# Kernel optimization log

Measured on AMD Instinct MI355X. Metric: run time of the kernel, lower is better.

The kernel has to match this reference:

```python
import jax, jax.numpy as jnp
import numpy as np

D = 1024
N_HEADS = 16


def build_masks(H, W):
    # Row-major grid: token i -> (i // W, i % W). True = attend.
    idx = jnp.arange(H * W)
    r, c = idx // W, idx % W
    ri, rj = r[:, None], r[None, :]
    ci, cj = c[:, None], c[None, :]
    lr = (ri > rj) | ((ri == rj) & (ci >= cj))
    rl = (ri < rj) | ((ri == rj) & (ci <= cj))
    td = (ci > cj) | ((ci == cj) & (ri >= rj))
    bu = (ci < cj) | ((ci == cj) & (ri <= rj))
    return lr, rl, td, bu


def dir_attn(x, w_qkv, w_o, mask):
    # x: (B,T,D); w_qkv: (3D,D); w_o: (D,D); mask: (T,T) bool
    B, T, Dm = x.shape
    hd = Dm // N_HEADS
    qkv = (x @ w_qkv.T).reshape(B, T, 3, N_HEADS, hd)
    q = qkv[:, :, 0].transpose(0, 2, 1, 3)  # (B,H,T,hd)
    k = qkv[:, :, 1].transpose(0, 2, 1, 3)
    v = qkv[:, :, 2].transpose(0, 2, 1, 3)
    scores = jnp.einsum('bhqd,bhkd->bhqk', q, k) / np.sqrt(hd)
    scores = jnp.where(mask[None, None], scores, -jnp.inf)
    attn = jax.nn.softmax(scores, axis=-1)
    y = jnp.einsum('bhqk,bhkd->bhqd', attn, v)
    y = y.transpose(0, 2, 1, 3).reshape(B, T, Dm)
    return y @ w_o.T


def rmsnorm(x, w, eps=1e-6):
    norm = jax.lax.rsqrt(jnp.mean(jnp.square(x.astype(jnp.float32)), axis=-1, keepdims=True) + eps)
    return (x.astype(jnp.float32) * norm).astype(x.dtype) * w


def setup_inputs() -> dict:
    key = jax.random.key(0)
    ks = jax.random.split(key, 13)
    s = 0.02
    inp = {
        'x': jax.random.normal(ks[0], (4, 1024, D), dtype=jnp.float32),
        'w_qkv_lr': jax.random.normal(ks[1], (3 * D, D), dtype=jnp.float32) * s,
        'w_o_lr':   jax.random.normal(ks[2], (D, D), dtype=jnp.float32) * s,
        'w_qkv_rl': jax.random.normal(ks[3], (3 * D, D), dtype=jnp.float32) * s,
        'w_o_rl':   jax.random.normal(ks[4], (D, D), dtype=jnp.float32) * s,
        'w_qkv_td': jax.random.normal(ks[5], (3 * D, D), dtype=jnp.float32) * s,
        'w_o_td':   jax.random.normal(ks[6], (D, D), dtype=jnp.float32) * s,
        'w_qkv_bu': jax.random.normal(ks[7], (3 * D, D), dtype=jnp.float32) * s,
        'w_o_bu':   jax.random.normal(ks[8], (D, D), dtype=jnp.float32) * s,
        'w_gate':   jax.random.normal(ks[9], (4 * D, 4 * D), dtype=jnp.float32) * s,
        'b_gate':   jnp.zeros((4 * D,), dtype=jnp.float32),
        'w_out':    jax.random.normal(ks[10], (D, 4 * D), dtype=jnp.float32) * s,
        'norm_w':   jnp.ones((D,), dtype=jnp.float32),
        'grid_h': 32,
        'grid_w': 32,
    }
    return inp


def reference(x, w_qkv_lr, w_o_lr, w_qkv_rl, w_o_rl, w_qkv_td, w_o_td,
              w_qkv_bu, w_o_bu, w_gate, b_gate, w_out, norm_w, grid_h, grid_w):
    m_lr, m_rl, m_td, m_bu = build_masks(grid_h, grid_w)
    h_lr = dir_attn(x, w_qkv_lr, w_o_lr, m_lr)
    h_rl = dir_attn(x, w_qkv_rl, w_o_rl, m_rl)
    h_td = dir_attn(x, w_qkv_td, w_o_td, m_td)
    h_bu = dir_attn(x, w_qkv_bu, w_o_bu, m_bu)
    concat = jnp.concatenate([h_lr, h_rl, h_td, h_bu], axis=-1)  # (B,T,4D)
    gate = jax.nn.sigmoid(concat @ w_gate.T + b_gate)
    fused = (gate * concat) @ w_out.T
    return rmsnorm(fused + x, norm_w)
```

## Files before the change

### kernel.cpp

```cpp
#include <hip/hip_runtime.h>
#include <hip/hip_bf16.h>
#include <math.h>


typedef __bf16 bf16_t;
typedef __bf16 bf16x4 __attribute__((ext_vector_type(4)));
typedef __bf16 bf16x8 __attribute__((ext_vector_type(8)));
typedef float  f32x4  __attribute__((ext_vector_type(4)));

#define MFMA16(a, b, c) __builtin_amdgcn_mfma_f32_16x16x32_bf16((a), (b), (c), 0, 0, 0)

__device__ __forceinline__ void async16(const bf16_t* g, bf16_t* l) {
  __builtin_amdgcn_global_load_lds((const __attribute__((address_space(1))) void*)g,
                                   (__attribute__((address_space(3))) void*)l,
                                   16, 0, 0);
}

__device__ __forceinline__ float dpp_max16(float x) {
  float t;
  t = __builtin_bit_cast(float, __builtin_amdgcn_update_dpp(0, __builtin_bit_cast(int, x), 0xB1, 0xF, 0xF, true));
  x = fmaxf(x, t);
  t = __builtin_bit_cast(float, __builtin_amdgcn_update_dpp(0, __builtin_bit_cast(int, x), 0x4E, 0xF, 0xF, true));
  x = fmaxf(x, t);
  t = __builtin_bit_cast(float, __builtin_amdgcn_update_dpp(0, __builtin_bit_cast(int, x), 0x124, 0xF, 0xF, true));
  x = fmaxf(x, t);
  t = __builtin_bit_cast(float, __builtin_amdgcn_update_dpp(0, __builtin_bit_cast(int, x), 0x128, 0xF, 0xF, true));
  x = fmaxf(x, t);
  return x;
}
__device__ __forceinline__ float dpp_sum16(float x) {
  float t;
  t = __builtin_bit_cast(float, __builtin_amdgcn_update_dpp(0, __builtin_bit_cast(int, x), 0xB1, 0xF, 0xF, true));
  x += t;
  t = __builtin_bit_cast(float, __builtin_amdgcn_update_dpp(0, __builtin_bit_cast(int, x), 0x4E, 0xF, 0xF, true));
  x += t;
  t = __builtin_bit_cast(float, __builtin_amdgcn_update_dpp(0, __builtin_bit_cast(int, x), 0x124, 0xF, 0xF, true));
  x += t;
  t = __builtin_bit_cast(float, __builtin_amdgcn_update_dpp(0, __builtin_bit_cast(int, x), 0x128, 0xF, 0xF, true));
  x += t;
  return x;
}

struct Ptr4 { const bf16_t* p[4]; };

__device__ __forceinline__ int perm_t(int p, int dir) {
  int q = (dir & 1) ? (1023 - p) : p;
  if (dir >= 2) q = ((q & 31) << 5) | (q >> 5);
  return q;
}

struct CvtDesc {
  const float* src[9];
  bf16_t* dst[9];
  int n8[9];
};

__device__ __forceinline__ void cvt8(const float* in, bf16_t* out, int i) {
  const float4 a = ((const float4*)in)[i * 2];
  const float4 b = ((const float4*)in)[i * 2 + 1];
  bf16x8 o;
  o[0] = (bf16_t)a.x; o[1] = (bf16_t)a.y; o[2] = (bf16_t)a.z; o[3] = (bf16_t)a.w;
  o[4] = (bf16_t)b.x; o[5] = (bf16_t)b.y; o[6] = (bf16_t)b.z; o[7] = (bf16_t)b.w;
  ((bf16x8*)out)[i] = o;
}

__global__ __launch_bounds__(256) void cvt9_k(CvtDesc d) {
  const int seg = blockIdx.y;
  const int i = blockIdx.x * 256 + threadIdx.x;
  if (i >= d.n8[seg]) return;
  cvt8(d.src[seg], d.dst[seg], i);
}

template <int MODE>
__global__ __launch_bounds__(512, 2) void gemm_bt2(
    const bf16_t* __restrict__ A, long sAz, int lda,
    Ptr4 B4, int ldb,
    void* __restrict__ Cv, long sCz, int ldc, int K, int koff,
    const float* __restrict__ bias,
    const bf16_t* __restrict__ gin,
    bf16_t* __restrict__ vtp, long sVz, int dirbase) {
  constexpr int BM = 256, BN = 256, BK = 64;
  (void)BM; (void)BN;
  __shared__ __align__(16) char smem[131072];

  const int z = blockIdx.z;
  const bf16_t* Ap = A + (long)z * sAz;
  const bf16_t* Bp = B4.p[z];
  const int tid = threadIdx.x;
  const int lane = tid & 63;
  const int wave = tid >> 6;
  const int l15 = lane & 15, qd = lane >> 4;
  const int wm = wave >> 2, wn = wave & 3;
  const int bm = blockIdx.y * 256, bn = blockIdx.x * 256;
  const int kz = (MODE == 3) ? z * koff : 0;
  const int NT = K / BK;

  const int row0 = tid >> 3;
  const int blkp = ((tid & 7) ^ (row0 & 7)) * 8;
  const bf16_t* gA = Ap + (long)(bm + row0) * lda + blkp + kz;
  const bf16_t* gB = Bp + (long)(bn + row0) * ldb + blkp + kz;
  char* const sm = (char*)smem;
  const int ldsT = tid * 16;

  const int xorv = (l15 & 7) << 4;
  const int aBase = (wm * 128 + l15) * 128;
  const int bBase = 32768 + (wn * 64 + l15) * 128;
  const int colk0 = (qd * 16) ^ xorv;
  const int colk1 = (64 + qd * 16) ^ xorv;

  f32x4 acc[8][4];
#pragma unroll
  for (int i = 0; i < 8; i++)
#pragma unroll
    for (int j = 0; j < 4; j++) acc[i][j] = (f32x4){0.f, 0.f, 0.f, 0.f};

#pragma unroll
  for (int u = 0; u < 4; u++)
    async16(gA + (long)(u * 64) * lda, (bf16_t*)(sm + u * 8192 + ldsT));
#pragma unroll
  for (int u = 0; u < 4; u++)
    async16(gB + (long)(u * 64) * ldb, (bf16_t*)(sm + 32768 + u * 8192 + ldsT));
  asm volatile("s_waitcnt vmcnt(0)" ::: "memory");
  __builtin_amdgcn_s_barrier();

  for (int kt = 0; kt < NT; ++kt) {
    const int c = kt & 1;
    const char* sa = sm + c * 65536;
    const int nb = (c ^ 1) * 65536;
    const long ko = (long)(kt + 1) * BK;
    bf16x8 bF[4][2];
#pragma unroll
    for (int p = 0; p < 4; ++p) {
      if (p == 0) {
#pragma unroll
        for (int n = 0; n < 4; ++n) {
          bF[n][0] = *(const bf16x8*)(sa + bBase + n * 2048 + colk0);
          bF[n][1] = *(const bf16x8*)(sa + bBase + n * 2048 + colk1);
        }
      }
      bf16x8 aF[2][2];
#pragma unroll
      for (int mm = 0; mm < 2; ++mm) {
        aF[mm][0] = *(const bf16x8*)(sa + aBase + (p * 2 + mm) * 2048 + colk0);
        aF[mm][1] = *(const bf16x8*)(sa + aBase + (p * 2 + mm) * 2048 + colk1);
      }
      if (kt + 1 < NT) {
        if (p == 0) {
#pragma unroll
          for (int u = 0; u < 4; u++)
            async16(gA + (long)(u * 64) * lda + ko,
                    (bf16_t*)(sm + nb + u * 8192 + ldsT));
        } else if (p == 1) {
#pragma unroll
          for (int u = 0; u < 4; u++)
            async16(gB + (long)(u * 64) * ldb + ko,
                    (bf16_t*)(sm + nb + 32768 + u * 8192 + ldsT));
        }
      }
      __builtin_amdgcn_s_barrier();
      asm volatile("s_waitcnt lgkmcnt(0)" ::: "memory");
      __builtin_amdgcn_s_setprio(1);
#pragma unroll
      for (int kh = 0; kh < 2; ++kh)
#pragma unroll
        for (int mm = 0; mm < 2; ++mm)
#pragma unroll
          for (int n = 0; n < 4; ++n)
            acc[p * 2 + mm][n] =
                MFMA16(aF[mm][kh], bF[n][kh], acc[p * 2 + mm][n]);
      __builtin_amdgcn_s_setprio(0);
      if (p == 3 && kt + 1 < NT)
        asm volatile("s_waitcnt vmcnt(0)" ::: "memory");
      __builtin_amdgcn_s_barrier();
    }
  }

  if constexpr (MODE == 4) {
    const int dir = dirbase + z;
    if (bn < 2048) {
      bf16_t* qkz = (bf16_t*)Cv + (long)z * sCz;
      const float ksc = (bn >= 1024) ? 0.125f : 1.0f;
      float* sC = (float*)smem;
#pragma unroll
      for (int p = 0; p < 4; ++p) {
        if (p) __syncthreads();
        if (wm == (p >> 1)) {
#pragma unroll
          for (int mm = 0; mm < 4; ++mm) {
            const int m = (p & 1) * 4 + mm;
#pragma unroll
            for (int n = 0; n < 4; ++n)
#pragma unroll
              for (int r = 0; r < 4; ++r)
                sC[(mm * 16 + qd * 4 + r) * 260 + wn * 64 + n * 16 + l15] =
                    acc[m][n][r];
          }
        }
        __syncthreads();
#pragma unroll
        for (int i = 0; i < 8; ++i) {
          const int idx = i * 512 + tid;
          const int rl = idx >> 6, c4 = (idx & 63) * 4;
          const float4 v4 = *(const float4*)&sC[rl * 260 + c4];
          const int grow = bm + p * 64 + rl;
          const int prow = (grow & ~1023) | perm_t(grow & 1023, dir);
          bf16x4 o;
          o[0] = (bf16_t)(v4.x * ksc); o[1] = (bf16_t)(v4.y * ksc);
          o[2] = (bf16_t)(v4.z * ksc); o[3] = (bf16_t)(v4.w * ksc);
          *(bf16x4*)(qkz + (long)prow * ldc + bn + c4) = o;
        }
      }
    } else if (dir < 2) {
      bf16_t* vz = vtp + (long)z * sVz;
      float* sCt = (float*)smem;
#pragma unroll
      for (int p = 0; p < 4; ++p) {
        if (p) __syncthreads();
        if (wm == (p >> 1)) {
#pragma unroll
          for (int mm = 0; mm < 4; ++mm) {
            const int m = (p & 1) * 4 + mm;
#pragma unroll
            for (int n = 0; n < 4; ++n)
#pragma unroll
              for (int r = 0; r < 4; ++r)
                sCt[(wn * 64 + n * 16 + l15) * 68 + mm * 16 + qd * 4 + r] =
                    acc[m][n][r];
          }
        }
        __syncthreads();
#pragma unroll
        for (int i = 0; i < 8; ++i) {
          const int idx = i * 512 + tid;
          const int col = idx >> 4, tq = idx & 15;
          const float4 v4 = *(const float4*)&sCt[col * 68 + tq * 4];
          const int t0 = (bm & 1023) + p * 64 + tq * 4;
          const int bb = bm >> 10;
          const int ch = bn + col - 2048;
          bf16_t* vrow =
              vz + (((long)bb * 16 + (ch >> 6)) * 64 + (ch & 63)) * 1024;
          if (dir == 0) {
            bf16x4 o;
            o[0] = (bf16_t)v4.x; o[1] = (bf16_t)v4.y;
            o[2] = (bf16_t)v4.z; o[3] = (bf16_t)v4.w;
            *(bf16x4*)(vrow + t0) = o;
          } else {
            bf16x4 o;
            o[0] = (bf16_t)v4.w; o[1] = (bf16_t)v4.z;
            o[2] = (bf16_t)v4.y; o[3] = (bf16_t)v4.x;
            *(bf16x4*)(vrow + (1020 - t0)) = o;
          }
        }
      }
    } else {
      bf16_t* vz = vtp + (long)z * sVz;
      bf16_t* sV = (bf16_t*)smem;
      const int bmm = bm & 1023;
      const int bb = bm >> 10;
      const int ub5 = ((dir & 1) ? (768 - bmm) : bmm) >> 5;
#pragma unroll
      for (int h = 0; h < 2; ++h) {
        if (h) __syncthreads();
        if ((wn >> 1) == h) {
          const int colB = (wn & 1) * 64;
#pragma unroll
          for (int m = 0; m < 8; ++m)
#pragma unroll
            for (int n = 0; n < 4; ++n)
#pragma unroll
              for (int r = 0; r < 4; ++r) {
                const int t = bmm + wm * 128 + m * 16 + qd * 4 + r;
                const int u = (dir & 1) ? (1023 - t) : t;
                const int cpi = (u & 31) * 8 + ((u >> 5) & 7);
                sV[(colB + n * 16 + l15) * 264 + cpi] = (bf16_t)acc[m][n][r];
              }
        }
        __syncthreads();
#pragma unroll
        for (int i = 0; i < 8; ++i) {
          const int idx = i * 512 + tid;
          const int col = idx >> 5, cg = idx & 31;
          const bf16x8 v = *(const bf16x8*)&sV[col * 264 + cg * 8];
          const int ch = bn + h * 128 + col - 2048;
          bf16_t* vrow =
              vz + (((long)bb * 16 + (ch >> 6)) * 64 + (ch & 63)) * 1024;
          *(bf16x8*)(vrow + cg * 32 + ub5) = v;
        }
      }
    }
  } else {
    float* sC = (float*)smem;
#pragma unroll
    for (int p = 0; p < 4; ++p) {
      if (p) __syncthreads();
      if (wm == (p >> 1)) {
#pragma unroll
        for (int mm = 0; mm < 4; ++mm) {
          const int m = (p & 1) * 4 + mm;
#pragma unroll
          for (int n = 0; n < 4; ++n)
#pragma unroll
            for (int r = 0; r < 4; ++r)
              sC[(mm * 16 + qd * 4 + r) * 260 + wn * 64 + n * 16 + l15] =
                  acc[m][n][r];
        }
      }
      __syncthreads();
#pragma unroll
      for (int i = 0; i < 8; ++i) {
        const int idx = i * 512 + tid;
        const int rl = idx >> 6, c4 = (idx & 63) * 4;
        const float4 v4 = *(const float4*)&sC[rl * 260 + c4];
        const int grow = bm + p * 64 + rl;
        const int gcol = bn + c4;
        const long goff = (long)grow * ldc + gcol;
        if constexpr (MODE == 0) {
          bf16x4 o;
          o[0] = (bf16_t)v4.x; o[1] = (bf16_t)v4.y;
          o[2] = (bf16_t)v4.z; o[3] = (bf16_t)v4.w;
          *(bf16x4*)((bf16_t*)Cv + (long)z * sCz + goff) = o;
        } else if constexpr (MODE == 1) {
          const float4 bb = *(const float4*)&bias[gcol];
          const bf16x4 gv = *(const bf16x4*)&gin[goff];
          bf16x4 o;
          o[0] = (bf16_t)((float)gv[0] / (1.f + __expf(-(v4.x + bb.x))));
          o[1] = (bf16_t)((float)gv[1] / (1.f + __expf(-(v4.y + bb.y))));
          o[2] = (bf16_t)((float)gv[2] / (1.f + __expf(-(v4.z + bb.z))));
          o[3] = (bf16_t)((float)gv[3] / (1.f + __expf(-(v4.w + bb.w))));
          *(bf16x4*)((bf16_t*)Cv + goff) = o;
        } else {
          *(float4*)((float*)Cv + (long)z * sCz + goff) = v4;
        }
      }
    }
  }
}

template <int MODE>
__global__ __launch_bounds__(256) void gemm_bt(
    const bf16_t* __restrict__ A, long sAz, int lda,
    Ptr4 B4, int ldb,
    void* __restrict__ Cv, long sCz, int ldc, int K, int koff,
    const float* __restrict__ bias,
    const bf16_t* __restrict__ gin,
    bf16_t* __restrict__ vtp, long sVz, int dirbase) {
  constexpr int BM = 128, BN = 128, BK = 32;
  __shared__ __align__(16) char smem[18432];
  bf16_t* sA = (bf16_t*)smem;
  bf16_t* sB = (bf16_t*)(smem + BM * BK * 2);
  float* sC = (float*)smem;

  const int z = blockIdx.z;
  const bf16_t* Ap = A + (long)z * sAz;
  const bf16_t* Bp = B4.p[z];
  const int tid = threadIdx.x;
  const int wave = tid >> 6, lane = tid & 63;
  const int lane15 = lane & 15, quad = lane >> 4;
  const int bm = blockIdx.y * BM, bn = blockIdx.x * BN;
  const int wm = (wave >> 1) * 64, wn = (wave & 1) * 64;

  f32x4 acc[4][4];
#pragma unroll
  for (int i = 0; i < 4; i++)
#pragma unroll
    for (int j = 0; j < 4; j++) acc[i][j] = (f32x4){0.f, 0.f, 0.f, 0.f};

  const int srow = wave * 16 + (lane >> 2);
  const int skoff = (lane & 3) * 8;
  const int kz = (MODE == 3) ? z * koff : 0;
  const bf16_t* ga = Ap + (long)(bm + srow) * lda + skoff + kz;
  const bf16_t* gb = Bp + (long)(bn + srow) * ldb + skoff + kz;
  bf16_t* la = &sA[srow * BK + skoff];
  bf16_t* lb = &sB[srow * BK + skoff];

  for (int k0 = 0; k0 < K; k0 += BK) {
    __syncthreads();
    async16(ga + k0, la);
    async16(ga + k0 + (long)64 * lda, la + 64 * BK);
    async16(gb + k0, lb);
    async16(gb + k0 + (long)64 * ldb, lb + 64 * BK);
    __syncthreads();

    bf16x8 af[4], bfv[4];
#pragma unroll
    for (int i = 0; i < 4; i++)
      af[i] = *(const bf16x8*)&sA[(wm + i * 16 + lane15) * BK + quad * 8];
#pragma unroll
    for (int j = 0; j < 4; j++)
      bfv[j] = *(const bf16x8*)&sB[(wn + j * 16 + lane15) * BK + quad * 8];
#pragma unroll
    for (int i = 0; i < 4; i++)
#pragma unroll
      for (int j = 0; j < 4; j++)
        acc[i][j] = MFMA16(af[i], bfv[j], acc[i][j]);
  }

  __syncthreads();

  if constexpr (MODE == 4) {
    const int dir = dirbase + z;
    if (bn < 2048) {
      bf16_t* qkz = (bf16_t*)Cv + (long)z * sCz;
      const float ksc = (bn >= 1024) ? 0.125f : 1.0f;
#pragma unroll
      for (int p = 0; p < 4; p++) {
        if (p) __syncthreads();
        const int sr = (wm >> 2) + quad * 4;
#pragma unroll
        for (int r = 0; r < 4; r++)
#pragma unroll
          for (int j = 0; j < 4; j++)
            sC[(sr + r) * 144 + wn + j * 16 + lane15] = acc[p][j][r];
        __syncthreads();
#pragma unroll
        for (int c = 0; c < 4; c++) {
          const int idx = c * 256 + tid;
          const int srr = idx >> 5, chunk = idx & 31;
          const float4 v4 = *(const float4*)&sC[srr * 144 + chunk * 4];
          const int grow = bm + p * 16 + (srr & 15) + (srr >> 4) * 64;
          const int prow = (grow & ~1023) | perm_t(grow & 1023, dir);
          bf16x4 o;
          o[0] = (bf16_t)(v4.x * ksc); o[1] = (bf16_t)(v4.y * ksc);
          o[2] = (bf16_t)(v4.z * ksc); o[3] = (bf16_t)(v4.w * ksc);
          *(bf16x4*)(qkz + (long)prow * 2048 + bn + chunk * 4) = o;
        }
      }
    } else {
      bf16_t* vz = vtp + (long)z * sVz;
      float* sCt = sC;
#pragma unroll
      for (int p = 0; p < 2; p++)
#pragma unroll
        for (int q = 0; q < 2; q++) {
          if (p || q) __syncthreads();
          if ((wave & 1) == q) {
#pragma unroll
            for (int ii = 0; ii < 2; ii++) {
              const int i = 2 * p + ii;
              const int srb = (wm >> 1) + ii * 16 + quad * 4;
#pragma unroll
              for (int r = 0; r < 4; r++)
#pragma unroll
                for (int j = 0; j < 4; j++)
                  sCt[(j * 16 + lane15) * 68 + srb + r] = acc[i][j][r];
            }
          }
          __syncthreads();
#pragma unroll
          for (int c = 0; c < 4; c++) {
            const int idx = c * 256 + tid;
            const int col = idx >> 4, tq = idx & 15;
            const int srr0 = (tq & 7) * 4 + (tq >> 3) * 32;
            const float4 v4 = *(const float4*)&sCt[col * 68 + srr0];
            const int t0 = (bm & 1023) + p * 32 + (srr0 & 31) + (srr0 >> 5) * 64;
            const int bb = bm >> 10;
            const int ch = bn + 64 * q + col - 2048;
            bf16_t* vrow =
                vz + (((long)bb * 16 + (ch >> 6)) * 64 + (ch & 63)) * 1024;
            if (dir == 0) {
              bf16x4 o;
              o[0] = (bf16_t)v4.x; o[1] = (bf16_t)v4.y;
              o[2] = (bf16_t)v4.z; o[3] = (bf16_t)v4.w;
              *(bf16x4*)(vrow + t0) = o;
            } else if (dir == 1) {
              bf16x4 o;
              o[0] = (bf16_t)v4.w; o[1] = (bf16_t)v4.z;
              o[2] = (bf16_t)v4.y; o[3] = (bf16_t)v4.x;
              *(bf16x4*)(vrow + (1020 - t0)) = o;
            } else {
              vrow[perm_t(t0 + 0, dir)] = (bf16_t)v4.x;
              vrow[perm_t(t0 + 1, dir)] = (bf16_t)v4.y;
              vrow[perm_t(t0 + 2, dir)] = (bf16_t)v4.z;
              vrow[perm_t(t0 + 3, dir)] = (bf16_t)v4.w;
            }
          }
        }
    }
  } else {
#pragma unroll
    for (int p = 0; p < 4; p++) {
      if (p) __syncthreads();
      const int sr = (wm >> 2) + quad * 4;
#pragma unroll
      for (int r = 0; r < 4; r++)
#pragma unroll
        for (int j = 0; j < 4; j++)
          sC[(sr + r) * 144 + wn + j * 16 + lane15] = acc[p][j][r];
      __syncthreads();
#pragma unroll
      for (int c = 0; c < 4; c++) {
        const int idx = c * 256 + tid;
        const int srr = idx >> 5, chunk = idx & 31;
        const float4 v4 = *(const float4*)&sC[srr * 144 + chunk * 4];
        const int grow = bm + p * 16 + (srr & 15) + (srr >> 4) * 64;
        const int gcol = bn + chunk * 4;
        const long goff = (long)grow * ldc + gcol;
        if constexpr (MODE == 0) {
          bf16x4 o;
          o[0] = (bf16_t)v4.x; o[1] = (bf16_t)v4.y;
          o[2] = (bf16_t)v4.z; o[3] = (bf16_t)v4.w;
          *(bf16x4*)((bf16_t*)Cv + (long)z * sCz + goff) = o;
        } else if constexpr (MODE == 1) {
          const float4 bb = *(const float4*)&bias[gcol];
          const bf16x4 gv = *(const bf16x4*)&gin[goff];
          bf16x4 o;
          o[0] = (bf16_t)((float)gv[0] / (1.f + __expf(-(v4.x + bb.x))));
          o[1] = (bf16_t)((float)gv[1] / (1.f + __expf(-(v4.y + bb.y))));
          o[2] = (bf16_t)((float)gv[2] / (1.f + __expf(-(v4.z + bb.z))));
          o[3] = (bf16_t)((float)gv[3] / (1.f + __expf(-(v4.w + bb.w))));
          *(bf16x4*)((bf16_t*)Cv + goff) = o;
        } else {
          *(float4*)((float*)Cv + (long)z * sCz + goff) = v4;
        }
      }
    }
  }
}

__global__ __launch_bounds__(256, 3) void attn_k(
    const bf16_t* __restrict__ qk, long sQz,
    const bf16_t* __restrict__ vt, long sVz,
    bf16_t* __restrict__ y, long sYz, int dir0) {
  const int p0 = blockIdx.y * 3 + blockIdx.x;
  const int chunk = (gridDim.y * 3) >> 3;
  const int lg = (p0 & 7) * chunk + (p0 >> 3);
  const int bx = lg % 3, by = lg / 3;
  const int zi = by >> 6;
  const int bh = by & 63;
  const int dir = dir0 + zi;
  const int b = bh >> 4, h = bh & 15;
  const int tid = threadIdx.x;
  const int wave = tid >> 6, lane = tid & 63;
  const int lane15 = lane & 15, quad = lane >> 4;
  const int hoff = h * 64;
  const bf16_t* base = qk + (long)zi * sQz + (long)b * 1024 * 2048;
  const bf16_t* vth = vt + (long)zi * sVz + ((long)b * 16 + h) * 64 * 1024;
  bf16_t* yd = y + (long)zi * sYz;

  __shared__ __align__(16) bf16_t sK[64 * 72];
  __shared__ __align__(16) bf16_t sVt[64 * 72];
  __shared__ __align__(16) bf16_t sP[4][32 * 72];

  const int krow = tid >> 3, kd = (tid & 7) * 8;
  const int vd = tid >> 2, pc = (tid & 3) * 8;
  const bf16_t* kb_g = base + 1024 + hoff;
  const float FNEG = -1e30f;

  const int np = (bx == 2) ? 4 : 2;
  for (int pass = 0; pass < np; ++pass) {
    const int qt = (bx == 0) ? (7 - 4 * pass)
                 : (bx == 1) ? (6 - 2 * pass)
                             : ((pass == 0) ? 5 : 3 - pass);

    bf16x8 qa[2][2];
#pragma unroll
    for (int g = 0; g < 2; g++) {
      const int row = qt * 128 + wave * 32 + g * 16 + lane15;
      qa[g][0] = *(const bf16x8*)(base + (long)row * 2048 + hoff + quad * 8);
      qa[g][1] = *(const bf16x8*)(base + (long)row * 2048 + hoff + 32 + quad * 8);
    }

    float mrow[2][4], lrow[2][4];
    f32x4 o[2][4];
#pragma unroll
    for (int g = 0; g < 2; g++)
#pragma unroll
      for (int r = 0; r < 4; r++) { mrow[g][r] = FNEG; lrow[g][r] = 0.f; }
#pragma unroll
    for (int g = 0; g < 2; g++)
#pragma unroll
      for (int d4 = 0; d4 < 4; d4++) o[g][d4] = (f32x4){0.f, 0.f, 0.f, 0.f};

    bf16x8 kA = *(const bf16x8*)(kb_g + (long)krow * 2048 + kd);
    bf16x8 kB = *(const bf16x8*)(kb_g + (long)(32 + krow) * 2048 + kd);
    bf16x8 vA = *(const bf16x8*)(vth + (long)vd * 1024 + pc);
    bf16x8 vB = *(const bf16x8*)(vth + (long)vd * 1024 + 32 + pc);

    const int qlo = qt * 128 + wave * 32;
    const int ktiles = 2 * qt + 2;
    for (int kt = 0; kt < ktiles; kt++) {
      __syncthreads();
      *(bf16x8*)&sK[krow * 72 + kd] = kA;
      *(bf16x8*)&sK[(krow + 32) * 72 + kd] = kB;
      *(bf16x8*)&sVt[vd * 72 + pc] = vA;
      *(bf16x8*)&sVt[vd * 72 + 32 + pc] = vB;
      __syncthreads();
      if (kt + 1 < ktiles) {
        const int nb = (kt + 1) * 64;
        kA = *(const bf16x8*)(kb_g + (long)(nb + krow) * 2048 + kd);
        kB = *(const bf16x8*)(kb_g + (long)(nb + 32 + krow) * 2048 + kd);
        vA = *(const bf16x8*)(vth + (long)vd * 1024 + nb + pc);
        vB = *(const bf16x8*)(vth + (long)vd * 1024 + nb + 32 + pc);
      }
      const int kbase = kt * 64;

      bf16x8 kb[4][2];
#pragma unroll
      for (int ns = 0; ns < 4; ns++) {
        kb[ns][0] = *(const bf16x8*)&sK[(ns * 16 + lane15) * 72 + quad * 8];
        kb[ns][1] = *(const bf16x8*)&sK[(ns * 16 + lane15) * 72 + 32 + quad * 8];
      }
      f32x4 s[2][4];
#pragma unroll
      for (int g = 0; g < 2; g++)
#pragma unroll
        for (int ns = 0; ns < 4; ns++) {
          f32x4 t = (f32x4){0.f, 0.f, 0.f, 0.f};
          t = MFMA16(qa[g][0], kb[ns][0], t);
          t = MFMA16(qa[g][1], kb[ns][1], t);
          s[g][ns] = t;
        }
      if (kbase + 63 > qlo) {
#pragma unroll
        for (int g = 0; g < 2; g++) {
          const int qc = qlo + g * 16 + quad * 4;
#pragma unroll
          for (int ns = 0; ns < 4; ns++) {
            const int kp = kbase + ns * 16 + lane15;
#pragma unroll
            for (int r = 0; r < 4; r++)
              if (kp > qc + r) s[g][ns][r] = FNEG;
          }
        }
      }
      float tm[2][4];
#pragma unroll
      for (int g = 0; g < 2; g++)
#pragma unroll
        for (int r = 0; r < 4; r++) {
          float t = fmaxf(fmaxf(s[g][0][r], s[g][1][r]),
                          fmaxf(s[g][2][r], s[g][3][r]));
          tm[g][r] = dpp_max16(t);
        }
      bool up = false;
#pragma unroll
      for (int g = 0; g < 2; g++)
#pragma unroll
        for (int r = 0; r < 4; r++) up = up || (tm[g][r] > mrow[g][r]);
      if (__any(up)) {
#pragma unroll
        for (int g = 0; g < 2; g++) {
          float alpha[4];
#pragma unroll
          for (int r = 0; r < 4; r++) {
            const float mn = fmaxf(mrow[g][r], tm[g][r]);
            alpha[r] = __expf(mrow[g][r] - mn);
            mrow[g][r] = mn;
          }
#pragma unroll
          for (int r = 0; r < 4; r++) lrow[g][r] *= alpha[r];
#pragma unroll
          for (int d4 = 0; d4 < 4; d4++)
#pragma unroll
            for (int r = 0; r < 4; r++) o[g][d4][r] *= alpha[r];
        }
      }
#pragma unroll
      for (int g = 0; g < 2; g++) {
#pragma unroll
        for (int ns = 0; ns < 4; ns++)
#pragma unroll
          for (int r = 0; r < 4; r++)
            s[g][ns][r] = __expf(s[g][ns][r] - mrow[g][r]);
#pragma unroll
        for (int r = 0; r < 4; r++) {
          float ts = (s[g][0][r] + s[g][1][r]) + (s[g][2][r] + s[g][3][r]);
          lrow[g][r] += dpp_sum16(ts);
        }
#pragma unroll
        for (int ns = 0; ns < 4; ns++)
#pragma unroll
          for (int r = 0; r < 4; r++)
            sP[wave][(g * 16 + quad * 4 + r) * 72 + ns * 16 + lane15] =
                (bf16_t)s[g][ns][r];
      }
      bf16x8 vb[4][2];
#pragma unroll
      for (int d4 = 0; d4 < 4; d4++) {
        vb[d4][0] = *(const bf16x8*)&sVt[(d4 * 16 + lane15) * 72 + quad * 8];
        vb[d4][1] = *(const bf16x8*)&sVt[(d4 * 16 + lane15) * 72 + 32 + quad * 8];
      }
#pragma unroll
      for (int g = 0; g < 2; g++) {
        const bf16x8 pa0 = *(const bf16x8*)&sP[wave][(g * 16 + lane15) * 72 + quad * 8];
        const bf16x8 pa1 = *(const bf16x8*)&sP[wave][(g * 16 + lane15) * 72 + 32 + quad * 8];
#pragma unroll
        for (int d4 = 0; d4 < 4; d4++) {
          o[g][d4] = MFMA16(pa0, vb[d4][0], o[g][d4]);
          o[g][d4] = MFMA16(pa1, vb[d4][1], o[g][d4]);
        }
      }
    }

#pragma unroll
    for (int g = 0; g < 2; g++)
#pragma unroll
      for (int r = 0; r < 4; r++) {
        const float rinv = 1.f / fmaxf(lrow[g][r], 1e-20f);
#pragma unroll
        for (int d4 = 0; d4 < 4; d4++)
          sP[wave][(g * 16 + quad * 4 + r) * 72 + d4 * 16 + lane15] =
              (bf16_t)(o[g][d4][r] * rinv);
      }
#pragma unroll
    for (int g = 0; g < 2; g++) {
      const bf16x8 o0 = *(const bf16x8*)&sP[wave][(g * 16 + lane15) * 72 + quad * 16];
      const bf16x8 o1 = *(const bf16x8*)&sP[wave][(g * 16 + lane15) * 72 + quad * 16 + 8];
      const int tok = perm_t(qt * 128 + wave * 32 + g * 16 + lane15, dir);
      bf16_t* yr = yd + ((long)b * 1024 + tok) * 1024 + hoff + quad * 16;
      *(bf16x8*)yr = o0;
      *(bf16x8*)(yr + 8) = o1;
    }
  }
}

__global__ __launch_bounds__(256) void rmsnorm_k(const float* __restrict__ p0,
                                                 const float* __restrict__ p1,
                                                 const float* __restrict__ p2,
                                                 const float* __restrict__ p3,
                                                 const float* __restrict__ x,
                                                 const float* __restrict__ w,
                                                 float* __restrict__ out) {
  const int row = blockIdx.x, tid = threadIdx.x;
  const long off = (long)row * 1024;
  const float4 a = ((const float4*)(p0 + off))[tid];
  const float4 bq = ((const float4*)(p1 + off))[tid];
  const float4 c = ((const float4*)(x + off))[tid];
  float4 v;
  v.x = a.x + bq.x + c.x;
  v.y = a.y + bq.y + c.y;
  v.z = a.z + bq.z + c.z;
  v.w = a.w + bq.w + c.w;
  if (p2) {
    const float4 d = ((const float4*)(p2 + off))[tid];
    const float4 e = ((const float4*)(p3 + off))[tid];
    v.x += d.x + e.x;
    v.y += d.y + e.y;
    v.z += d.z + e.z;
    v.w += d.w + e.w;
  }
  float ss = v.x * v.x + v.y * v.y + v.z * v.z + v.w * v.w;
#pragma unroll
  for (int o2 = 32; o2 >= 1; o2 >>= 1) ss += __shfl_xor(ss, o2);
  __shared__ float wsum[4];
  if ((tid & 63) == 0) wsum[tid >> 6] = ss;
  __syncthreads();
  const float tot = wsum[0] + wsum[1] + wsum[2] + wsum[3];
  const float norm = rsqrtf(tot * (1.f / 1024.f) + 1e-6f);
  const float4 wv = ((const float4*)w)[tid];
  v.x = v.x * norm * wv.x;
  v.y = v.y * norm * wv.y;
  v.z = v.z * norm * wv.z;
  v.w = v.w * norm * wv.w;
  ((float4*)(out + off))[tid] = v;
}

extern "C" void kernel_launch(void* const* d_in, const int* in_sizes, int n_in,
                              void* d_out, int out_size, void* d_ws, size_t ws_size,
                              hipStream_t stream) {
  (void)in_sizes; (void)n_in; (void)out_size;
  const float* xf = (const float*)d_in[0];
  const float* wqkv_f[4] = {(const float*)d_in[1], (const float*)d_in[3],
                            (const float*)d_in[5], (const float*)d_in[7]};
  const float* wo_f[4] = {(const float*)d_in[2], (const float*)d_in[4],
                          (const float*)d_in[6], (const float*)d_in[8]};
  const float* wgate_f = (const float*)d_in[9];
  const float* bgate_f = (const float*)d_in[10];
  const float* wout_f = (const float*)d_in[11];
  const float* normw_f = (const float*)d_in[12];

  const long MB = 1l << 20;
  char* ws = (char*)d_ws;
  const dim3 blk(256);
  const dim3 blk2(512);
  const bool batched = ws_size >= (size_t)(168 * MB);
  const long sQK = 4096l * 2048;
  const long sVT = 4096l * 1024;
  const long sY  = 4096l * 1024;

  if (batched) {
    bf16_t* x_c    = (bf16_t*)(ws);
    bf16_t* wq_c   = (bf16_t*)(ws + 8 * MB);
    bf16_t* wo_c   = (bf16_t*)(ws + 32 * MB);
    bf16_t* qk     = (bf16_t*)(ws + 40 * MB);
    bf16_t* vt     = (bf16_t*)(ws + 104 * MB);
    bf16_t* y      = (bf16_t*)(ws + 136 * MB);
    bf16_t* concat = (bf16_t*)(ws + 40 * MB);
    bf16_t* wg_c   = (bf16_t*)(ws + 72 * MB);
    bf16_t* wout_c = (bf16_t*)(ws);
    float*  part4  = (float*)(ws + 40 * MB);
    bf16_t* gated  = y;

    {
      CvtDesc cd;
      cd.src[0] = xf; cd.dst[0] = x_c; cd.n8[0] = 4194304 / 8;
      for (int d = 0; d < 4; d++) {
        cd.src[1 + d] = wqkv_f[d];
        cd.dst[1 + d] = wq_c + (long)d * 3145728;
        cd.n8[1 + d] = 3145728 / 8;
        cd.src[5 + d] = wo_f[d];
        cd.dst[5 + d] = wo_c + (long)d * 1048576;
        cd.n8[5 + d] = 1048576 / 8;
      }
      cvt9_k<<<dim3(2048, 9), blk, 0, stream>>>(cd);
    }
    {
      Ptr4 bq{{wq_c, wq_c + 3145728, wq_c + 2l * 3145728, wq_c + 3l * 3145728}};
      gemm_bt2<4><<<dim3(12, 16, 4), blk2, 0, stream>>>(
          x_c, 0, 1024, bq, 1024, qk, sQK, 2048, 1024, 0, nullptr, nullptr,
          vt, sVT, 0);
    }
    attn_k<<<dim3(3, 256), blk, 0, stream>>>(qk, sQK, vt, sVT, y, sY, 0);
    {
      CvtDesc cd;
      for (int s = 0; s < 9; s++) cd.n8[s] = 0;
      cd.src[0] = wgate_f; cd.dst[0] = wg_c; cd.n8[0] = 16777216 / 8;
      cd.src[1] = wout_f; cd.dst[1] = wout_c; cd.n8[1] = 4194304 / 8;
      cvt9_k<<<dim3(8192, 2), blk, 0, stream>>>(cd);
    }
    {
      Ptr4 b4{{wo_c, wo_c + 1048576, wo_c + 2097152, wo_c + 3145728}};
      gemm_bt2<0><<<dim3(4, 16, 4), blk2, 0, stream>>>(
          y, sY, 1024, b4, 1024, concat, 1024, 4096, 1024, 0, nullptr, nullptr,
          nullptr, 0, 0);
    }
    {
      Ptr4 b4{{wg_c, wg_c, wg_c, wg_c}};
      gemm_bt2<1><<<dim3(16, 16, 1), blk2, 0, stream>>>(
          concat, 0, 4096, b4, 4096, gated, 0, 4096, 4096, 0, bgate_f, concat,
          nullptr, 0, 0);
    }
    {
      Ptr4 b4{{wout_c, wout_c, wout_c, wout_c}};
      gemm_bt2<3><<<dim3(4, 16, 4), blk2, 0, stream>>>(
          gated, 0, 4096, b4, 4096, part4, (long)4096 * 1024, 1024, 1024, 1024,
          nullptr, nullptr, nullptr, 0, 0);
    }
    rmsnorm_k<<<dim3(4096), blk, 0, stream>>>(
        part4, part4 + (long)4096 * 1024, part4 + 2l * 4096 * 1024,
        part4 + 3l * 4096 * 1024, xf, normw_f, (float*)d_out);
  } else {
    bf16_t* x_c    = (bf16_t*)(ws);
    bf16_t* wq_c   = (bf16_t*)(ws + 8 * MB);
    bf16_t* qk_d   = (bf16_t*)(ws + 32 * MB);
    bf16_t* vt_d   = (bf16_t*)(ws + 48 * MB);
    bf16_t* wo_c   = (bf16_t*)(ws + 56 * MB);
    bf16_t* y      = (bf16_t*)(ws + 64 * MB);
    bf16_t* concat = (bf16_t*)(ws);
    bf16_t* wg_c   = (bf16_t*)(ws + 32 * MB);
    bf16_t* wout_c = (bf16_t*)(ws);
    float*  part   = (float*)(ws + 8 * MB);
    bf16_t* gated  = y;

    {
      CvtDesc cd;
      cd.src[0] = xf; cd.dst[0] = x_c; cd.n8[0] = 4194304 / 8;
      for (int d = 0; d < 4; d++) {
        cd.src[1 + d] = wqkv_f[d];
        cd.dst[1 + d] = wq_c + (long)d * 3145728;
        cd.n8[1 + d] = 3145728 / 8;
        cd.src[5 + d] = wo_f[d];
        cd.dst[5 + d] = wo_c + (long)d * 1048576;
        cd.n8[5 + d] = 1048576 / 8;
      }
      cvt9_k<<<dim3(2048, 9), blk, 0, stream>>>(cd);
    }
    for (int d = 0; d < 4; d++) {
      const bf16_t* wq_d = wq_c + (long)d * 3145728;
      Ptr4 bq{{wq_d, wq_d, wq_d, wq_d}};
      gemm_bt<4><<<dim3(24, 32, 1), blk, 0, stream>>>(
          x_c, 0, 1024, bq, 1024, qk_d, 0, 2048, 1024, 0, nullptr, nullptr,
          vt_d, 0, d);
      attn_k<<<dim3(3, 64), blk, 0, stream>>>(qk_d, 0, vt_d, 0,
                                              y + (long)d * sY, 0, d);
    }
    {
      Ptr4 b4{{wo_c, wo_c + 1048576, wo_c + 2097152, wo_c + 3145728}};
      gemm_bt<0><<<dim3(8, 32, 4), blk, 0, stream>>>(
          y, sY, 1024, b4, 1024, concat, 1024, 4096, 1024, 0, nullptr, nullptr,
          nullptr, 0, 0);
    }
    {
      CvtDesc cd;
      for (int s = 0; s < 9; s++) cd.n8[s] = 0;
      cd.src[0] = wgate_f; cd.dst[0] = wg_c; cd.n8[0] = 16777216 / 8;
      cvt9_k<<<dim3(8192, 1), blk, 0, stream>>>(cd);
    }
    {
      Ptr4 b4{{wg_c, wg_c, wg_c, wg_c}};
      gemm_bt<1><<<dim3(32, 32, 1), blk, 0, stream>>>(
          concat, 0, 4096, b4, 4096, gated, 0, 4096, 4096, 0, bgate_f, concat,
          nullptr, 0, 0);
    }
    {
      CvtDesc cd;
      for (int s = 0; s < 9; s++) cd.n8[s] = 0;
      cd.src[0] = wout_f; cd.dst[0] = wout_c; cd.n8[0] = 4194304 / 8;
      cvt9_k<<<dim3(2048, 1), blk, 0, stream>>>(cd);
    }
    {
      Ptr4 b4{{wout_c, wout_c, wout_c, wout_c}};
      gemm_bt<3><<<dim3(8, 32, 2), blk, 0, stream>>>(
          gated, 0, 4096, b4, 4096, part, (long)4096 * 1024, 1024, 2048, 2048,
          nullptr, nullptr, nullptr, 0, 0);
    }
    rmsnorm_k<<<dim3(4096), blk, 0, stream>>>(part, part + (long)4096 * 1024,
                                              nullptr, nullptr,
                                              xf, normw_f, (float*)d_out);
  }
}
```

Measured before the change: 605.9 us.

## Switch GEMM mainloop to 4-stage BK=32 pipeline with rotated LDS swizzle

Replaces the double-buffered BK=64 main loop of the shared 256x256 GEMM with a four-slot ring of BK=32 stages, keeping three stages of global-to-LDS async loads in flight and using staged vmcnt waits. The LDS layout moves from 128-byte rows with an XOR swizzle to 64-byte rows with a rotation-based permutation chosen to avoid bank conflicts. The aim is to hide global memory latency better. The cost is more barriers per unit of K and more complex wait-count bookkeeping; correctness depends on the counts matching the number of loads issued.

Result: slower. 655.0 us (+8.1%).

```diff
diff --git a/kernel.cpp b/kernel.cpp
--- a/kernel.cpp
+++ b/kernel.cpp
@@ -79,8 +79,6 @@
     const float* __restrict__ bias,
     const bf16_t* __restrict__ gin,
     bf16_t* __restrict__ vtp, long sVz, int dirbase) {
-  constexpr int BM = 256, BN = 256, BK = 64;
-  (void)BM; (void)BN;
   __shared__ __align__(16) char smem[131072];
 
   const int z = blockIdx.z;
@@ -93,20 +91,33 @@
   const int wm = wave >> 2, wn = wave & 3;
   const int bm = blockIdx.y * 256, bn = blockIdx.x * 256;
   const int kz = (MODE == 3) ? z * koff : 0;
-  const int NT = K / BK;
-
-  const int row0 = tid >> 3;
-  const int blkp = ((tid & 7) ^ (row0 & 7)) * 8;
-  const bf16_t* gA = Ap + (long)(bm + row0) * lda + blkp + kz;
-  const bf16_t* gB = Bp + (long)(bn + row0) * ldb + blkp + kz;
+  const int NS = K / 32;
+
+  const int srow = tid >> 2;
+  const int sblk = tid & 3;
+  const int sg = ((sblk - srow - (srow >> 2)) & 3) * 8;
+  const bf16_t* gA = Ap + (long)(bm + srow) * lda + sg + kz;
+  const bf16_t* gB = Bp + (long)(bn + srow) * ldb + sg + kz;
+  const long ldA128 = (long)128 * lda, ldB128 = (long)128 * ldb;
   char* const sm = (char*)smem;
   const int ldsT = tid * 16;
 
-  const int xorv = (l15 & 7) << 4;
-  const int aBase = (wm * 128 + l15) * 128;
-  const int bBase = 32768 + (wn * 64 + l15) * 128;
-  const int colk0 = (qd * 16) ^ xorv;
-  const int colk1 = (64 + qd * 16) ^ xorv;
+#define STAGE_A(t)                                                        \
+  {                                                                       \
+    char* bb_ = sm + (((t) & 3) << 15);                                   \
+    const int ko_ = (t) * 32;                                             \
+    async16(gA + ko_, (bf16_t*)(bb_ + ldsT));                             \
+    async16(gA + ko_ + ldA128, (bf16_t*)(bb_ + 8192 + ldsT));             \
+  }
+#define STAGE_B(t)                                                        \
+  {                                                                       \
+    char* bb_ = sm + (((t) & 3) << 15);                                   \
+    const int ko_ = (t) * 32;                                             \
+    async16(gB + ko_, (bf16_t*)(bb_ + 16384 + ldsT));                     \
+    async16(gB + ko_ + ldB128, (bf16_t*)(bb_ + 24576 + ldsT));            \
+  }
+
+  const int lf = l15 + (l15 >> 2);
 
   f32x4 acc[8][4];
 #pragma unroll
@@ -114,66 +125,63 @@
 #pragma unroll
     for (int j = 0; j < 4; j++) acc[i][j] = (f32x4){0.f, 0.f, 0.f, 0.f};
 
-#pragma unroll
-  for (int u = 0; u < 4; u++)
-    async16(gA + (long)(u * 64) * lda, (bf16_t*)(sm + u * 8192 + ldsT));
-#pragma unroll
-  for (int u = 0; u < 4; u++)
-    async16(gB + (long)(u * 64) * ldb, (bf16_t*)(sm + 32768 + u * 8192 + ldsT));
-  asm volatile("s_waitcnt vmcnt(0)" ::: "memory");
+  STAGE_A(0) STAGE_B(0) STAGE_A(1) STAGE_B(1) STAGE_A(2) STAGE_B(2)
+  asm volatile("s_waitcnt vmcnt(8)" ::: "memory");
   __builtin_amdgcn_s_barrier();
 
-  for (int kt = 0; kt < NT; ++kt) {
-    const int c = kt & 1;
-    const char* sa = sm + c * 65536;
-    const int nb = (c ^ 1) * 65536;
-    const long ko = (long)(kt + 1) * BK;
-    bf16x8 bF[4][2];
-#pragma unroll
-    for (int p = 0; p < 4; ++p) {
-      if (p == 0) {
-#pragma unroll
-        for (int n = 0; n < 4; ++n) {
-          bF[n][0] = *(const bf16x8*)(sa + bBase + n * 2048 + colk0);
-          bF[n][1] = *(const bf16x8*)(sa + bBase + n * 2048 + colk1);
-        }
-      }
-      bf16x8 aF[2][2];
-#pragma unroll
-      for (int mm = 0; mm < 2; ++mm) {
-        aF[mm][0] = *(const bf16x8*)(sa + aBase + (p * 2 + mm) * 2048 + colk0);
-        aF[mm][1] = *(const bf16x8*)(sa + aBase + (p * 2 + mm) * 2048 + colk1);
-      }
-      if (kt + 1 < NT) {
-        if (p == 0) {
-#pragma unroll
-          for (int u = 0; u < 4; u++)
-            async16(gA + (long)(u * 64) * lda + ko,
-                    (bf16_t*)(sm + nb + u * 8192 + ldsT));
-        } else if (p == 1) {
-#pragma unroll
-          for (int u = 0; u < 4; u++)
-            async16(gB + (long)(u * 64) * ldb + ko,
-                    (bf16_t*)(sm + nb + 32768 + u * 8192 + ldsT));
-        }
-      }
-      __builtin_amdgcn_s_barrier();
-      asm volatile("s_waitcnt lgkmcnt(0)" ::: "memory");
-      __builtin_amdgcn_s_setprio(1);
-#pragma unroll
-      for (int kh = 0; kh < 2; ++kh)
-#pragma unroll
-        for (int mm = 0; mm < 2; ++mm)
-#pragma unroll
-          for (int n = 0; n < 4; ++n)
-            acc[p * 2 + mm][n] =
-                MFMA16(aF[mm][kh], bF[n][kh], acc[p * 2 + mm][n]);
-      __builtin_amdgcn_s_setprio(0);
-      if (p == 3 && kt + 1 < NT)
-        asm volatile("s_waitcnt vmcnt(0)" ::: "memory");
-      __builtin_amdgcn_s_barrier();
-    }
+  for (int s = 0; s < NS; ++s) {
+    const char* sb = sm + ((s & 3) << 15);
+    bf16x8 bF[4], aF[4];
+#pragma unroll
+    for (int n = 0; n < 4; ++n) {
+      const int R = wn * 64 + n * 16 + l15;
+      const int f = (qd + lf + wn * 80 + n * 20) & 3;
+      bF[n] = *(const bf16x8*)(sb + 16384 + R * 64 + (f << 4));
+    }
+#pragma unroll
+    for (int m = 0; m < 4; ++m) {
+      const int R = wm * 128 + m * 16 + l15;
+      const int f = (qd + lf + wm * 160 + m * 20) & 3;
+      aF[m] = *(const bf16x8*)(sb + R * 64 + (f << 4));
+    }
+    if (s + 3 < NS) STAGE_A(s + 3)
+    __builtin_amdgcn_s_barrier();
+    asm volatile("s_waitcnt lgkmcnt(0)" ::: "memory");
+    __builtin_amdgcn_s_setprio(1);
+#pragma unroll
+    for (int m = 0; m < 4; ++m)
+#pragma unroll
+      for (int n = 0; n < 4; ++n)
+        acc[m][n] = MFMA16(aF[m], bF[n], acc[m][n]);
+    __builtin_amdgcn_s_setprio(0);
+    __builtin_amdgcn_s_barrier();
+#pragma unroll
+    for (int m = 0; m < 4; ++m) {
+      const int R = wm * 128 + (m + 4) * 16 + l15;
+      const int f = (qd + lf + wm * 160 + (m + 4) * 20) & 3;
+      aF[m] = *(const bf16x8*)(sb + R * 64 + (f << 4));
+    }
+    if (s + 3 < NS) STAGE_B(s + 3)
+    __builtin_amdgcn_s_barrier();
+    asm volatile("s_waitcnt lgkmcnt(0)" ::: "memory");
+    __builtin_amdgcn_s_setprio(1);
+#pragma unroll
+    for (int m = 0; m < 4; ++m)
+#pragma unroll
+      for (int n = 0; n < 4; ++n)
+        acc[m + 4][n] = MFMA16(aF[m], bF[n], acc[m + 4][n]);
+    __builtin_amdgcn_s_setprio(0);
+    const int rem = NS - 1 - s;
+    if (rem >= 3)
+      asm volatile("s_waitcnt vmcnt(8)" ::: "memory");
+    else if (rem == 2)
+      asm volatile("s_waitcnt vmcnt(4)" ::: "memory");
+    else if (rem == 1)
+      asm volatile("s_waitcnt vmcnt(0)" ::: "memory");
+    __builtin_amdgcn_s_barrier();
   }
+#undef STAGE_A
+#undef STAGE_B
 
   if constexpr (MODE == 4) {
     const int dir = dirbase + z;
```
